# Kernel tuning notes

Measured on AMD Instinct MI355X. Metric: run time of the kernel, lower is better.

The kernel has to match this reference:

```python
import jax, jax.numpy as jnp
import numpy as np

H = 1024          # hidden_size
K = 128           # MAX_LINK_CANDIDATES (cap applies to both keys and values)
EPS = 1e-8


def _spatial_features(kb, vb):
    """kb: [B,K,4] key boxes, vb: [B,V,4] value boxes -> [B,K,V,8].
    Vectorized version of _compute_spatial_features_pair over all (key,value) pairs."""
    kcx = (kb[..., 0] + kb[..., 2]) / 2
    kcy = (kb[..., 1] + kb[..., 3]) / 2
    vcx = (vb[..., 0] + vb[..., 2]) / 2
    vcy = (vb[..., 1] + vb[..., 3]) / 2
    dx = vcx[:, None, :] - kcx[:, :, None]                      # [B,K,V]
    dy = vcy[:, None, :] - kcy[:, :, None]
    dist = jnp.sqrt(dx ** 2 + dy ** 2 + EPS)
    angle = jnp.arctan2(dy, dx)
    kh = kb[..., 3] - kb[..., 1]
    vh = vb[..., 3] - vb[..., 1]
    h_ov = jnp.clip(jnp.minimum(kb[..., 3][:, :, None], vb[..., 3][:, None, :])
                    - jnp.maximum(kb[..., 1][:, :, None], vb[..., 1][:, None, :]), 0)
    h_align = h_ov / (jnp.minimum(kh[:, :, None], vh[:, None, :]) + EPS)
    kw = kb[..., 2] - kb[..., 0]
    vw = vb[..., 2] - vb[..., 0]
    v_ov = jnp.clip(jnp.minimum(kb[..., 2][:, :, None], vb[..., 2][:, None, :])
                    - jnp.maximum(kb[..., 0][:, :, None], vb[..., 0][:, None, :]), 0)
    v_align = v_ov / (jnp.minimum(kw[:, :, None], vw[:, None, :]) + EPS)
    area_ratio = (vh * vw)[:, None, :] / ((kh * kw)[:, :, None] + EPS)
    aspect = (vw / (vh + EPS))[:, None, :] / ((kw / (kh + EPS))[:, :, None])
    return jnp.stack([dx, dy, dist, angle, h_align, v_align, area_ratio, aspect], axis=-1)


def setup_inputs() -> dict:
    key = jax.random.key(0)
    ks = jax.random.split(key, 20)
    B, S = 4, 2048
    sequence_output = jax.random.normal(ks[0], (B, S, H), dtype=jnp.float32)
    entity_logits = jax.random.normal(ks[1], (B, S, 3), dtype=jnp.float32)
    base = jax.random.uniform(ks[2], (B, S, 2), dtype=jnp.float32) * 0.9
    size = jax.random.uniform(ks[3], (B, S, 2), dtype=jnp.float32) * 0.09 + 0.01
    bboxes = jnp.concatenate([base, base + size], axis=-1)      # valid x1<x2, y1<y2
    attention_mask = jnp.ones((B, S), dtype=jnp.int32)
    s = 1.0 / np.sqrt(H)
    inp = {
        "sequence_output": sequence_output,
        "entity_logits": entity_logits,
        "bboxes": bboxes,
        "attention_mask": attention_mask,
        "Wk": jax.random.normal(ks[4], (H, H), jnp.float32) * s,
        "bk": jnp.zeros((H,), jnp.float32),
        "Wv": jax.random.normal(ks[5], (H, H), jnp.float32) * s,
        "bv": jnp.zeros((H,), jnp.float32),
        "Wbil": jax.random.normal(ks[6], (H, H), jnp.float32) * s,   # bilinear weight (out=1 squeezed)
        "bbil": jnp.zeros((), jnp.float32),
        "Ws1": jax.random.normal(ks[7], (8, 64), jnp.float32) * (1.0 / np.sqrt(8)),
        "bs1": jnp.zeros((64,), jnp.float32),
        "Ws2": jax.random.normal(ks[8], (64, 32), jnp.float32) * (1.0 / np.sqrt(64)),
        "bs2": jnp.zeros((32,), jnp.float32),
        "Wf1": jax.random.normal(ks[9], (33, 16), jnp.float32) * (1.0 / np.sqrt(33)),
        "bf1": jnp.zeros((16,), jnp.float32),
        "Wf2": jax.random.normal(ks[10], (16, 1), jnp.float32) * 0.25,
        "bf2": jnp.zeros((1,), jnp.float32),
    }
    return inp


def reference(sequence_output, entity_logits, bboxes, attention_mask,
              Wk, bk, Wv, bv, Wbil, bbil, Ws1, bs1, Ws2, bs2, Wf1, bf1, Wf2, bf2):
    # Candidate selection: top-K tokens by class confidence among predicted keys/values.
    probs = jax.nn.softmax(entity_logits, axis=-1)
    preds = jnp.argmax(entity_logits, axis=-1)                  # [B,S]
    valid = attention_mask == 1
    key_conf = jnp.where((preds == 1) & valid, probs[..., 1], -jnp.inf)
    val_conf = jnp.where((preds == 2) & valid, probs[..., 2], -jnp.inf)
    _, key_idx = jax.lax.top_k(key_conf, K)                     # [B,K]
    _, val_idx = jax.lax.top_k(val_conf, K)

    seq_k = jnp.take_along_axis(sequence_output, key_idx[..., None], axis=1)  # [B,K,H]
    seq_v = jnp.take_along_axis(sequence_output, val_idx[..., None], axis=1)
    key_reps = seq_k @ Wk + bk                                  # dropout is identity at eval
    val_reps = seq_v @ Wv + bv

    # Bilinear scoring: k^T W v  -> [B,K,V] (chunking in torch is a memory detail, same math)
    biaffine = jnp.einsum('bkh,hg,bvg->bkv', key_reps, Wbil, val_reps) + bbil

    key_boxes = jnp.take_along_axis(bboxes, key_idx[..., None], axis=1)       # [B,K,4]
    val_boxes = jnp.take_along_axis(bboxes, val_idx[..., None], axis=1)
    sf = _spatial_features(key_boxes, val_boxes)                              # [B,K,V,8]
    spatial = jax.nn.relu(sf @ Ws1 + bs1) @ Ws2 + bs2                         # [B,K,V,32]

    combined = jnp.concatenate([biaffine[..., None], spatial], axis=-1)       # [B,K,V,33]
    scores = (jax.nn.relu(combined @ Wf1 + bf1) @ Wf2 + bf2)[..., 0]          # [B,K,V]
    return scores, key_idx, val_idx
```

## Files before the change

### kernel.cpp

```cpp
#include <hip/hip_runtime.h>
#include <hip/hip_bf16.h>
#include <math.h>

#define B_ 4
#define S_ 2048
#define H_ 1024
#define KC 128
#define EPSF 1e-8f

typedef __attribute__((ext_vector_type(8))) short bf16x8;
typedef __attribute__((ext_vector_type(4))) float f32x4;

static __device__ inline unsigned short f2b(float f) {
    unsigned u = __float_as_uint(f);
    return (unsigned short)((u + 0x7fffu + ((u >> 16) & 1u)) >> 16);
}

static __device__ inline unsigned long long shflx64(unsigned long long v, int m) {
    int lo = __shfl_xor((int)(unsigned)(v & 0xffffffffull), m, 64);
    int hi = __shfl_xor((int)(unsigned)(v >> 32), m, 64);
    return ((unsigned long long)(unsigned)hi << 32) | (unsigned)lo;
}

#define CROSS_STAGE(k, j) do {                                              \
    const int lm = (j) >> 3;                                                \
    const bool upL  = (((lane) * 8) & (k)) == 0;                            \
    const bool lowr = ((lane) & lm) == 0;                                   \
    _Pragma("unroll")                                                       \
    for (int r = 0; r < 8; ++r) {                                           \
        unsigned long long o = shflx64(e[r], lm);                           \
        e[r] = ((upL == lowr) == (e[r] < o)) ? e[r] : o;                    \
    }                                                                       \
} while (0)

#define INTRA_STAGE(j, k) do {                                              \
    _Pragma("unroll")                                                       \
    for (int r = 0; r < 8; ++r) if (!(r & (j))) {                           \
        bool up = ((((lane) * 8 + r) & (k)) == 0);                          \
        unsigned long long a = e[r], b = e[r | (j)];                        \
        if (up ? (a > b) : (a < b)) { e[r] = b; e[r | (j)] = a; }           \
    }                                                                       \
} while (0)

static __device__ inline void wave_sort512(unsigned long long e[8], int lane) {
    INTRA_STAGE(1, 2);
    INTRA_STAGE(2, 4);  INTRA_STAGE(1, 4);
    INTRA_STAGE(4, 8);  INTRA_STAGE(2, 8);  INTRA_STAGE(1, 8);
    CROSS_STAGE(16, 8);
    INTRA_STAGE(4, 16); INTRA_STAGE(2, 16); INTRA_STAGE(1, 16);
    CROSS_STAGE(32, 16); CROSS_STAGE(32, 8);
    INTRA_STAGE(4, 32); INTRA_STAGE(2, 32); INTRA_STAGE(1, 32);
    CROSS_STAGE(64, 32); CROSS_STAGE(64, 16); CROSS_STAGE(64, 8);
    INTRA_STAGE(4, 64); INTRA_STAGE(2, 64); INTRA_STAGE(1, 64);
    CROSS_STAGE(128, 64); CROSS_STAGE(128, 32); CROSS_STAGE(128, 16);
    CROSS_STAGE(128, 8);
    INTRA_STAGE(4, 128); INTRA_STAGE(2, 128); INTRA_STAGE(1, 128);
    CROSS_STAGE(256, 128); CROSS_STAGE(256, 64); CROSS_STAGE(256, 32);
    CROSS_STAGE(256, 16); CROSS_STAGE(256, 8);
    INTRA_STAGE(4, 256); INTRA_STAGE(2, 256); INTRA_STAGE(1, 256);
    CROSS_STAGE(512, 256); CROSS_STAGE(512, 128); CROSS_STAGE(512, 64);
    CROSS_STAGE(512, 32); CROSS_STAGE(512, 16); CROSS_STAGE(512, 8);
    INTRA_STAGE(4, 512); INTRA_STAGE(2, 512); INTRA_STAGE(1, 512);
}

static __device__ inline void topk_block(
    const float* logits, const int* mask, int blk,
    int* key_idx, int* val_idx, float* out_idx_base,
    unsigned long long* cand, int tid)
{
    const int b   = blk >> 1;
    const int cls = (blk & 1) ? 2 : 1;
    const int wv = tid >> 6, lane = tid & 63;
    unsigned long long e[8];
    #pragma unroll
    for (int r = 0; r < 8; ++r) {
        int s = wv * 512 + lane * 8 + r;
        float l0 = logits[(b * S_ + s) * 3 + 0];
        float l1 = logits[(b * S_ + s) * 3 + 1];
        float l2 = logits[(b * S_ + s) * 3 + 2];
        int pred = 0; float bl = l0;
        if (l1 > bl) { bl = l1; pred = 1; }
        if (l2 > bl) { bl = l2; pred = 2; }
        float c = -1.0f;
        if (pred == cls && mask[b * S_ + s] == 1) {
            double m = (double)bl;
            double e0 = exp((double)l0 - m);
            double e1 = exp((double)l1 - m);
            double e2 = exp((double)l2 - m);
            c = (float)(((cls == 1) ? e1 : e2) / (e0 + e1 + e2));
        }
        unsigned int u = __float_as_uint(c);
        unsigned int mono = (u & 0x80000000u) ? ~u : (u | 0x80000000u);
        e[r] = ((unsigned long long)(~mono) << 32) | (unsigned int)s;
    }
    wave_sort512(e, lane);
    if (lane < 16) {
        #pragma unroll
        for (int r = 0; r < 8; ++r) cand[wv * 128 + lane * 8 + r] = e[r];
    }
    __syncthreads();
    if (wv == 0) {
        #pragma unroll
        for (int r = 0; r < 8; ++r) e[r] = cand[lane * 8 + r];
        wave_sort512(e, lane);
        if (lane < 16) {
            int* idx_out = (blk & 1) ? (val_idx + b * KC) : (key_idx + b * KC);
            float* oidx  = out_idx_base + ((blk & 1) ? B_ * KC : 0) + b * KC;
            #pragma unroll
            for (int r = 0; r < 8; ++r) {
                int sel = (int)(e[r] & 0xffffffffu);
                idx_out[lane * 8 + r] = sel;
                oidx[lane * 8 + r] = (float)sel;
            }
        }
    }
}

__global__ __launch_bounds__(256) void prep_kernel(
    const float* __restrict__ Wk, const float* __restrict__ Wv,
    const float* __restrict__ Wbil, unsigned short* __restrict__ Wt,
    const float* __restrict__ logits, const int* __restrict__ mask,
    int* __restrict__ key_idx, int* __restrict__ val_idx,
    float* __restrict__ out_idx)
{
    __shared__ float tile[32][33];
    __shared__ unsigned long long cand[512];
    const int tid = threadIdx.x;
    if (blockIdx.x < 3072) {
        const int z = blockIdx.x >> 10;
        const int remb = blockIdx.x & 1023;
        const float* Win = (z == 0) ? Wk : (z == 1) ? Wv : Wbil;
        unsigned short* out = Wt + (size_t)z * H_ * H_;
        const int n0 = (remb & 31) * 32, k0 = (remb >> 5) * 32;
        const int r = tid >> 3, c0 = (tid & 7) * 4;
        float4 v = *(const float4*)(Win + (size_t)(k0 + r) * H_ + n0 + c0);
        tile[r][c0 + 0] = v.x; tile[r][c0 + 1] = v.y;
        tile[r][c0 + 2] = v.z; tile[r][c0 + 3] = v.w;
        __syncthreads();
        short4 o;
        o.x = (short)f2b(tile[c0 + 0][r]);
        o.y = (short)f2b(tile[c0 + 1][r]);
        o.z = (short)f2b(tile[c0 + 2][r]);
        o.w = (short)f2b(tile[c0 + 3][r]);
        *(short4*)(out + (size_t)(n0 + r) * H_ + k0 + c0) = o;
        return;
    }
    topk_block(logits, mask, blockIdx.x - 3072, key_idx, val_idx, out_idx,
               cand, tid);
}

__global__ __launch_bounds__(256) void gatherconv_kernel(
    const float* __restrict__ seq,
    const int* __restrict__ key_idx, const int* __restrict__ val_idx,
    unsigned short* __restrict__ Abf)
{
    const int row = blockIdx.x;
    const int tid = threadIdx.x;
    int b, srow;
    if (row < 512) { b = row >> 7; srow = key_idx[row]; }
    else           { b = (row - 512) >> 7; srow = val_idx[row - 512]; }
    const float* src = seq + ((size_t)b * S_ + srow) * H_ + tid * 4;
    float4 v = *(const float4*)src;
    short4 o;
    o.x = (short)f2b(v.x); o.y = (short)f2b(v.y);
    o.z = (short)f2b(v.z); o.w = (short)f2b(v.w);
    *(short4*)(Abf + (size_t)row * H_ + tid * 4) = o;
}

__global__ __launch_bounds__(256) void gemm_lds_kernel(
    const unsigned short* __restrict__ Ab,
    const unsigned short* __restrict__ Wt,
    const float* __restrict__ b0, const float* __restrict__ b1,
    unsigned short* __restrict__ Cout)
{
    __shared__ __align__(16) char As[32 * 256];
    __shared__ __align__(16) char Bs[64 * 256];

    const int NW8 = gridDim.x >> 3;
    int sw = ((int)blockIdx.x & 7) * NW8 + ((int)blockIdx.x >> 3);
    const int z  = sw >> 8;
    const int r2 = sw & 255;
    const int n0 = (r2 >> 4) * 64;
    const int m0 = (r2 & 15) * 32;

    Ab   += (size_t)z * 512 * H_;
    Cout += (size_t)z * 512 * H_;
    const unsigned short* Wz = Wt + (size_t)z * H_ * H_;
    const float* bias = z ? b1 : b0;

    const int tid  = threadIdx.x;
    const int lane = tid & 63, wv = tid >> 6;
    const int r = lane & 15, kq = (lane >> 4) * 8;

    const int srow = tid >> 3, sch = tid & 7;

    f32x4 acc[2] = {};

    for (int k0 = 0; k0 < H_; k0 += 128) {
        {
            bf16x8 va = *(const bf16x8*)(Ab + (size_t)(m0 + srow) * H_
                                         + k0 + sch * 8);
            *(bf16x8*)(As + srow * 256 + ((sch ^ (srow & 7)) << 4)) = va;
            #pragma unroll
            for (int p = 0; p < 2; ++p) {
                int rb = p * 32 + srow;
                bf16x8 vb = *(const bf16x8*)(Wz + (size_t)(n0 + rb) * H_
                                             + k0 + sch * 8);
                *(bf16x8*)(Bs + rb * 256 + ((sch ^ (rb & 7)) << 4)) = vb;
            }
        }
        __syncthreads();
        #pragma unroll
        for (int kk = 0; kk < 4; ++kk) {
            const int chv = ((kk * 32 + kq) >> 3) ^ (r & 7);
            bf16x8 av0 = *(const bf16x8*)(As + r * 256 + (chv << 4));
            bf16x8 av1 = *(const bf16x8*)(As + (16 + r) * 256 + (chv << 4));
            bf16x8 bv  = *(const bf16x8*)(Bs + (wv * 16 + r) * 256 + (chv << 4));
            acc[0] = __builtin_amdgcn_mfma_f32_16x16x32_bf16(av0, bv, acc[0], 0, 0, 0);
            acc[1] = __builtin_amdgcn_mfma_f32_16x16x32_bf16(av1, bv, acc[1], 0, 0, 0);
        }
        __syncthreads();
    }

    const int orow = (lane >> 4) * 4, ocol = lane & 15;
    const int n = n0 + wv * 16 + ocol;
    const float bv_ = bias ? bias[n] : 0.0f;
    #pragma unroll
    for (int i = 0; i < 2; ++i)
        #pragma unroll
        for (int g = 0; g < 4; ++g)
            Cout[(size_t)(m0 + i * 16 + orow + g) * H_ + n] = f2b(acc[i][g] + bv_);
}

__global__ __launch_bounds__(512) void biasp_kernel(
    const unsigned short* __restrict__ kbt,
    const unsigned short* __restrict__ vrep,
    const float* __restrict__ bbil, const float* __restrict__ bboxes,
    const int* __restrict__ key_idx, const int* __restrict__ val_idx,
    const float* __restrict__ Ws1, const float* __restrict__ bs1,
    const float* __restrict__ Ws2, const float* __restrict__ bs2,
    const float* __restrict__ Wf1, const float* __restrict__ bf1,
    const float* __restrict__ Wf2, const float* __restrict__ bf2,
    float* __restrict__ out)
{
    __shared__ float part[8][16][16];
    __shared__ float4 sWs1T[128];
    __shared__ float  sbs1[64];
    __shared__ float4 sWs2v[512];
    __shared__ float4 sbs2v[8];
    __shared__ float  sWf1c0[16];
    __shared__ float4 sWf1v[128];
    __shared__ float  sbf1[16];
    __shared__ float  sWf2[16];

    const int tid = threadIdx.x;
    for (int i = tid; i < 128; i += 512) {
        int j = i >> 1, q = i & 1;
        sWs1T[i] = (float4){Ws1[(4*q+0)*64+j], Ws1[(4*q+1)*64+j],
                            Ws1[(4*q+2)*64+j], Ws1[(4*q+3)*64+j]};
    }
    for (int i = tid; i < 64;  i += 512) sbs1[i] = bs1[i];
    if (tid < 512) sWs2v[tid] = ((const float4*)Ws2)[tid];
    if (tid < 8)  sbs2v[tid] = ((const float4*)bs2)[tid];
    if (tid < 16) sWf1c0[tid] = Wf1[tid];
    for (int i = tid; i < 128; i += 512) {
        int t = i >> 3, q = i & 7;
        sWf1v[i] = (float4){Wf1[(1+4*q+0)*16+t], Wf1[(1+4*q+1)*16+t],
                            Wf1[(1+4*q+2)*16+t], Wf1[(1+4*q+3)*16+t]};
    }
    if (tid < 16) sbf1[tid] = bf1[tid];
    if (tid < 16) sWf2[tid] = Wf2[tid];

    const int b = blockIdx.x >> 6;
    const int t = blockIdx.x & 63;
    const int m0 = (t >> 3) * 16, n0 = (t & 7) * 16;
    const int lane = tid & 63, wv = tid >> 6;
    const int r = lane & 15, kq = (lane >> 4) * 8;

    f32x4 acc = {};
    const unsigned short* a0 = kbt  + (size_t)(b * KC + m0 + r) * H_ + kq;
    const unsigned short* w0 = vrep + (size_t)(b * KC + n0 + r) * H_ + kq;
    #pragma unroll
    for (int kk = 0; kk < 4; ++kk) {
        int k0 = wv * 128 + kk * 32;
        acc = __builtin_amdgcn_mfma_f32_16x16x32_bf16(
            *(const bf16x8*)(a0 + k0), *(const bf16x8*)(w0 + k0), acc, 0, 0, 0);
    }
    const int orow = (lane >> 4) * 4, ocol = lane & 15;
    #pragma unroll
    for (int g = 0; g < 4; ++g) part[wv][orow + g][ocol] = acc[g];
    __syncthreads();

    if (tid >= 256) return;

    const int kl = tid >> 4, vl = tid & 15;
    float c0 = bbil[0];
    #pragma unroll
    for (int w = 0; w < 8; ++w) c0 += part[w][kl][vl];
    const int kg = m0 + kl, vg = n0 + vl;

    const float* kbx = bboxes + ((size_t)b * S_ + key_idx[b * KC + kg]) * 4;
    const float* vbx = bboxes + ((size_t)b * S_ + val_idx[b * KC + vg]) * 4;
    float k0_ = kbx[0], k1_ = kbx[1], k2_ = kbx[2], k3_ = kbx[3];
    float v0_ = vbx[0], v1_ = vbx[1], v2_ = vbx[2], v3_ = vbx[3];

    float kcx = (k0_ + k2_) * 0.5f, kcy = (k1_ + k3_) * 0.5f;
    float vcx = (v0_ + v2_) * 0.5f, vcy = (v1_ + v3_) * 0.5f;
    float dx = vcx - kcx, dy = vcy - kcy;
    float dist = sqrtf(dx * dx + dy * dy + EPSF);
    float angle = atan2f(dy, dx);
    float kh = k3_ - k1_, vh = v3_ - v1_, kw = k2_ - k0_, vw = v2_ - v0_;
    float h_ov = fmaxf(fminf(k3_, v3_) - fmaxf(k1_, v1_), 0.0f);
    float h_align = h_ov / (fminf(kh, vh) + EPSF);
    float v_ov = fmaxf(fminf(k2_, v2_) - fmaxf(k0_, v0_), 0.0f);
    float v_align = v_ov / (fminf(kw, vw) + EPSF);
    float area_ratio = (vh * vw) / (kh * kw + EPSF);
    float aspect = (vw / (vh + EPSF)) / (kw / (kh + EPSF));

    float4 sfa = {dx, dy, dist, angle};
    float4 sfb = {h_align, v_align, area_ratio, aspect};

    float4 h2v[8];
    #pragma unroll
    for (int q = 0; q < 8; ++q) h2v[q] = sbs2v[q];
    for (int j = 0; j < 64; ++j) {
        float4 w1a = sWs1T[j * 2], w1b = sWs1T[j * 2 + 1];
        float a = sbs1[j]
                + sfa.x * w1a.x + sfa.y * w1a.y + sfa.z * w1a.z + sfa.w * w1a.w
                + sfb.x * w1b.x + sfb.y * w1b.y + sfb.z * w1b.z + sfb.w * w1b.w;
        a = fmaxf(a, 0.0f);
        const float4* w2 = &sWs2v[j * 8];
        #pragma unroll
        for (int q = 0; q < 8; ++q) {
            float4 w = w2[q];
            h2v[q].x += a * w.x; h2v[q].y += a * w.y;
            h2v[q].z += a * w.z; h2v[q].w += a * w.w;
        }
    }
    float score = bf2[0];
    for (int tt = 0; tt < 16; ++tt) {
        float f = sbf1[tt] + c0 * sWf1c0[tt];
        const float4* w = &sWf1v[tt * 8];
        #pragma unroll
        for (int q = 0; q < 8; ++q) {
            float4 ww = w[q];
            f += h2v[q].x * ww.x + h2v[q].y * ww.y
               + h2v[q].z * ww.z + h2v[q].w * ww.w;
        }
        score += fmaxf(f, 0.0f) * sWf2[tt];
    }
    out[((size_t)b * KC + kg) * KC + vg] = score;
}

extern "C" void kernel_launch(void* const* d_in, const int* in_sizes, int n_in,
                              void* d_out, int out_size, void* d_ws, size_t ws_size,
                              hipStream_t stream) {
    const float* seq    = (const float*)d_in[0];
    const float* logits = (const float*)d_in[1];
    const float* bboxes = (const float*)d_in[2];
    const int*   mask   = (const int*)d_in[3];
    const float* Wk   = (const float*)d_in[4];
    const float* bk   = (const float*)d_in[5];
    const float* Wv   = (const float*)d_in[6];
    const float* bv   = (const float*)d_in[7];
    const float* Wbil = (const float*)d_in[8];
    const float* bbil = (const float*)d_in[9];
    const float* Ws1  = (const float*)d_in[10];
    const float* bs1  = (const float*)d_in[11];
    const float* Ws2  = (const float*)d_in[12];
    const float* bs2  = (const float*)d_in[13];
    const float* Wf1  = (const float*)d_in[14];
    const float* bf1  = (const float*)d_in[15];
    const float* Wf2  = (const float*)d_in[16];
    const float* bf2  = (const float*)d_in[17];

    float* out = (float*)d_out;
    char* ws = (char*)d_ws;

    int* key_idx = (int*)(ws + 64);
    int* val_idx = key_idx + B_ * KC;
    unsigned short* Wt   = (unsigned short*)(ws + 8192);
    unsigned short* Abf  = Wt + (size_t)3 * H_ * H_;
    unsigned short* reps = Abf + (size_t)1024 * H_;
    unsigned short* kbt  = reps + (size_t)1024 * H_;

    prep_kernel<<<3080, 256, 0, stream>>>(Wk, Wv, Wbil, Wt,
                                          logits, mask, key_idx, val_idx,
                                          out + B_ * KC * KC);
    gatherconv_kernel<<<1024, 256, 0, stream>>>(seq, key_idx, val_idx, Abf);
    gemm_lds_kernel<<<512, 256, 0, stream>>>(Abf, Wt, bk, bv, reps);
    gemm_lds_kernel<<<256, 256, 0, stream>>>(
        reps, Wt + (size_t)2 * H_ * H_, nullptr, nullptr, kbt);
    biasp_kernel<<<256, 512, 0, stream>>>(kbt, reps + (size_t)512 * H_,
                                          bbil, bboxes, key_idx, val_idx,
                                          Ws1, bs1, Ws2, bs2,
                                          Wf1, bf1, Wf2, bf2, out);
}
```

Before: 73.64 us.

## Enlarge GEMM block tile to 64x64 with 2x2 warp sub-tiles and K-step 256

New measurement: 76.43 us. +3.8%, slower.

```diff
diff --git a/kernel.cpp b/kernel.cpp
--- a/kernel.cpp
+++ b/kernel.cpp
@@ -173,15 +173,15 @@
     const float* __restrict__ b0, const float* __restrict__ b1,
     unsigned short* __restrict__ Cout)
 {
-    __shared__ __align__(16) char As[32 * 256];
-    __shared__ __align__(16) char Bs[64 * 256];
+    __shared__ __align__(16) char As[64 * 512];
+    __shared__ __align__(16) char Bs[64 * 512];
 
     const int NW8 = gridDim.x >> 3;
     int sw = ((int)blockIdx.x & 7) * NW8 + ((int)blockIdx.x >> 3);
-    const int z  = sw >> 8;
-    const int r2 = sw & 255;
-    const int n0 = (r2 >> 4) * 64;
-    const int m0 = (r2 & 15) * 32;
+    const int z  = sw >> 7;
+    const int r2 = sw & 127;
+    const int n0 = (r2 >> 3) * 64;
+    const int m0 = (r2 & 7) * 64;
 
     Ab   += (size_t)z * 512 * H_;
     Cout += (size_t)z * 512 * H_;
@@ -190,46 +190,66 @@
 
     const int tid  = threadIdx.x;
     const int lane = tid & 63, wv = tid >> 6;
-    const int r = lane & 15, kq = (lane >> 4) * 8;
-
-    const int srow = tid >> 3, sch = tid & 7;
-
-    f32x4 acc[2] = {};
-
-    for (int k0 = 0; k0 < H_; k0 += 128) {
-        {
-            bf16x8 va = *(const bf16x8*)(Ab + (size_t)(m0 + srow) * H_
-                                         + k0 + sch * 8);
-            *(bf16x8*)(As + srow * 256 + ((sch ^ (srow & 7)) << 4)) = va;
+    const int r = lane & 15, g = lane >> 4;
+    const int mh = (wv >> 1) * 32, nh = (wv & 1) * 32;
+
+    const int prow = tid >> 4;
+    const int pch  = tid & 15;
+
+    f32x4 acc[2][2] = {};
+
+    for (int k0 = 0; k0 < H_; k0 += 256) {
+        #pragma unroll
+        for (int p = 0; p < 4; ++p) {
+            const int row = p * 16 + prow;
+            const unsigned short* ag = Ab + (size_t)(m0 + row) * H_ + k0;
+            const unsigned short* bg = Wz + (size_t)(n0 + row) * H_ + k0;
+            bf16x8 a0 = *(const bf16x8*)(ag + pch * 8);
+            bf16x8 a1 = *(const bf16x8*)(ag + (pch + 16) * 8);
+            bf16x8 v0 = *(const bf16x8*)(bg + pch * 8);
+            bf16x8 v1 = *(const bf16x8*)(bg + (pch + 16) * 8);
+            *(bf16x8*)(As + row * 512 + ((pch ^ (row & 7)) << 4)) = a0;
+            *(bf16x8*)(As + row * 512 + (((pch + 16) ^ (row & 7)) << 4)) = a1;
+            *(bf16x8*)(Bs + row * 512 + ((pch ^ (row & 7)) << 4)) = v0;
+            *(bf16x8*)(Bs + row * 512 + (((pch + 16) ^ (row & 7)) << 4)) = v1;
+        }
+        __syncthreads();
+        #pragma unroll
+        for (int kk = 0; kk < 8; ++kk) {
+            const int c = kk * 4 + g;
+            bf16x8 av[2], bv[2];
             #pragma unroll
-            for (int p = 0; p < 2; ++p) {
-                int rb = p * 32 + srow;
-                bf16x8 vb = *(const bf16x8*)(Wz + (size_t)(n0 + rb) * H_
-                                             + k0 + sch * 8);
-                *(bf16x8*)(Bs + rb * 256 + ((sch ^ (rb & 7)) << 4)) = vb;
+            for (int i = 0; i < 2; ++i) {
+                const int row = mh + i * 16 + r;
+                av[i] = *(const bf16x8*)(As + row * 512 + ((c ^ (row & 7)) << 4));
             }
+            #pragma unroll
+            for (int j = 0; j < 2; ++j) {
+                const int row = nh + j * 16 + r;
+                bv[j] = *(const bf16x8*)(Bs + row * 512 + ((c ^ (row & 7)) << 4));
+            }
+            #pragma unroll
+            for (int i = 0; i < 2; ++i)
+                #pragma unroll
+                for (int j = 0; j < 2; ++j)
+                    acc[i][j] = __builtin_amdgcn_mfma_f32_16x16x32_bf16(
+                        av[i], bv[j], acc[i][j], 0, 0, 0);
         }
         __syncthreads();
-        #pragma unroll
-        for (int kk = 0; kk < 4; ++kk) {
-            const int chv = ((kk * 32 + kq) >> 3) ^ (r & 7);
-            bf16x8 av0 = *(const bf16x8*)(As + r * 256 + (chv << 4));
-            bf16x8 av1 = *(const bf16x8*)(As + (16 + r) * 256 + (chv << 4));
-            bf16x8 bv  = *(const bf16x8*)(Bs + (wv * 16 + r) * 256 + (chv << 4));
-            acc[0] = __builtin_amdgcn_mfma_f32_16x16x32_bf16(av0, bv, acc[0], 0, 0, 0);
-            acc[1] = __builtin_amdgcn_mfma_f32_16x16x32_bf16(av1, bv, acc[1], 0, 0, 0);
-        }
-        __syncthreads();
     }
 
     const int orow = (lane >> 4) * 4, ocol = lane & 15;
-    const int n = n0 + wv * 16 + ocol;
-    const float bv_ = bias ? bias[n] : 0.0f;
     #pragma unroll
     for (int i = 0; i < 2; ++i)
         #pragma unroll
-        for (int g = 0; g < 4; ++g)
-            Cout[(size_t)(m0 + i * 16 + orow + g) * H_ + n] = f2b(acc[i][g] + bv_);
+        for (int j = 0; j < 2; ++j) {
+            const int n = n0 + nh + j * 16 + ocol;
+            const float bv_ = bias ? bias[n] : 0.0f;
+            #pragma unroll
+            for (int gg = 0; gg < 4; ++gg)
+                Cout[(size_t)(m0 + mh + i * 16 + orow + gg) * H_ + n]
+                    = f2b(acc[i][j][gg] + bv_);
+        }
 }
 
 __global__ __launch_bounds__(512) void biasp_kernel(
@@ -388,8 +408,8 @@
                                           logits, mask, key_idx, val_idx,
                                           out + B_ * KC * KC);
     gatherconv_kernel<<<1024, 256, 0, stream>>>(seq, key_idx, val_idx, Abf);
-    gemm_lds_kernel<<<512, 256, 0, stream>>>(Abf, Wt, bk, bv, reps);
-    gemm_lds_kernel<<<256, 256, 0, stream>>>(
+    gemm_lds_kernel<<<256, 256, 0, stream>>>(Abf, Wt, bk, bv, reps);
+    gemm_lds_kernel<<<128, 256, 0, stream>>>(
         reps, Wt + (size_t)2 * H_ * H_, nullptr, nullptr, kbt);
     biasp_kernel<<<256, 512, 0, stream>>>(kbt, reps + (size_t)512 * H_,
                                           bbil, bboxes, key_idx, val_idx,
```
